# Kernel optimization log

Measured on AMD Instinct MI355X. Metric: run time of the kernel, lower is better.

Reference implementation:

```python
import jax, jax.numpy as jnp
import numpy as np

D = 256; HEADS = 8; DH = 32; LVLS = 3; PTS = 4; FF = 1024; FCD = 12544
SHAPES = ((100, 152), (50, 76), (25, 38))  # stride 8/16/32 maps for an 800x1216 image
INCH = (512, 1024, 2048)
N = 2; P_IMG = 1000


def sine_pos(h, w):
    # PositionEmbeddingSine, normalize=True, fully-valid mask
    eps = 1e-6; scale = 2.0 * np.pi
    y = jnp.cumsum(jnp.ones((h, w), jnp.float32), 0)
    x = jnp.cumsum(jnp.ones((h, w), jnp.float32), 1)
    y = y / (y[-1:, :] + eps) * scale
    x = x / (x[:, -1:] + eps) * scale
    dim_t = 10000.0 ** ((2.0 * (jnp.arange(128) // 2)).astype(jnp.float32) / 128.0)
    def inter(p):  # interleave sin/cos like torch.stack(...).flatten(3)
        return jnp.stack([jnp.sin(p[..., 0::2]), jnp.cos(p[..., 1::2])], -1).reshape(h, w, 128)
    return jnp.concatenate([inter(y[..., None] / dim_t), inter(x[..., None] / dim_t)], -1).reshape(h * w, D)


def bilinear(img, gx, gy):
    # F.grid_sample bilinear, align_corners=False, padding_mode='zeros'
    # img [C,H,W]; gx,gy in [-1,1] of any shape -> out [C, *gx.shape]
    C, H, W = img.shape
    x = ((gx + 1.0) * W - 1.0) * 0.5
    y = ((gy + 1.0) * H - 1.0) * 0.5
    x0 = jnp.floor(x); y0 = jnp.floor(y)
    wx = x - x0; wy = y - y0
    x0i = x0.astype(jnp.int32); y0i = y0.astype(jnp.int32)
    def g(xi, yi):
        ok = ((xi >= 0) & (xi < W) & (yi >= 0) & (yi < H)).astype(img.dtype)
        v = img[:, jnp.clip(yi, 0, H - 1), jnp.clip(xi, 0, W - 1)]
        return v * ok[None]
    return (g(x0i, y0i) * ((1 - wx) * (1 - wy))[None]
            + g(x0i + 1, y0i) * (wx * (1 - wy))[None]
            + g(x0i, y0i + 1) * ((1 - wx) * wy)[None]
            + g(x0i + 1, y0i + 1) * (wx * wy)[None])


def layernorm(x, g, b):
    mu = x.mean(-1, keepdims=True)
    var = ((x - mu) ** 2).mean(-1, keepdims=True)
    return (x - mu) / jnp.sqrt(var + 1e-5) * g + b


def _forward(feat0, feat1, feat2, point_coords, projw, projb, gng, gnb, level_embed,
             w_off, b_off, w_attn, b_attn, w_val, b_val, w_out, b_out,
             ln1_g, ln1_b, ln2_g, ln2_b, w_ff1, b_ff1, w_ff2, b_ff2, fc_w, fc_b):
    feats = (feat0, feat1, feat2)
    srcs = []; poss = []
    for l in range(LVLS):
        # input_proj: 1x1 conv + GroupNorm(32, 256)
        s = jnp.einsum('nchw,oc->nohw', feats[l], projw[l]) + projb[l][None, :, None, None]
        n, c, h, w = s.shape
        sg = s.reshape(n, 32, c // 32, h, w)
        mu = sg.mean((2, 3, 4), keepdims=True)
        var = ((sg - mu) ** 2).mean((2, 3, 4), keepdims=True)
        s = ((sg - mu) / jnp.sqrt(var + 1e-5)).reshape(n, c, h, w) * gng[l][None, :, None, None] + gnb[l][None, :, None, None]
        srcs.append(s.reshape(n, c, h * w).transpose(0, 2, 1))
        poss.append(sine_pos(h, w)[None] + level_embed[l][None, None, :])
    src = jnp.concatenate(srcs, 1)            # [N, Len, D]
    pos = jnp.concatenate(poss, 1)            # [1, Len, D] broadcast
    # reference points (valid_ratios == 1)
    refs = []
    for (h, w) in SHAPES:
        gy, gx = jnp.meshgrid((jnp.arange(h) + 0.5) / h, (jnp.arange(w) + 0.5) / w, indexing='ij')
        refs.append(jnp.stack([gx.ravel(), gy.ravel()], -1))
    ref = jnp.concatenate(refs, 0)            # [Len, 2] (x, y)
    Lq = src.shape[1]
    q = src + pos
    value = (src @ w_val.T + b_val).reshape(N, Lq, HEADS, DH)
    off = (q @ w_off.T + b_off).reshape(N, Lq, HEADS, LVLS, PTS, 2)
    aw = jax.nn.softmax((q @ w_attn.T + b_attn).reshape(N, Lq, HEADS, LVLS * PTS), -1).reshape(N, Lq, HEADS, LVLS, PTS)
    norm = jnp.array([[w, h] for (h, w) in SHAPES], jnp.float32)  # [L, 2] offset normalizer (W_, H_)
    locs = ref[None, :, None, None, None, :] + off / norm[None, None, None, :, None, :]  # [N,Lq,H,L,P,2]
    # MSDeformAttn core: per-level bilinear gather, accumulate weighted samples
    acc = jnp.zeros((N * HEADS, DH, Lq), src.dtype)
    start = 0
    for lvl, (h, w) in enumerate(SHAPES):
        v = value[:, start:start + h * w].transpose(0, 2, 3, 1).reshape(N * HEADS, DH, h, w)
        g = (2.0 * locs[:, :, :, lvl] - 1.0).transpose(0, 2, 1, 3, 4).reshape(N * HEADS, Lq, PTS, 2)
        s = jax.vmap(bilinear)(v, g[..., 0], g[..., 1])                 # [NH, DH, Lq, PTS]
        a = aw[:, :, :, lvl].transpose(0, 2, 1, 3).reshape(N * HEADS, 1, Lq, PTS)
        acc = acc + (s * a).sum(-1)
        start += h * w
    attn_out = acc.reshape(N, HEADS * DH, Lq).transpose(0, 2, 1) @ w_out.T + b_out
    x = layernorm(src + attn_out, ln1_g, ln1_b)
    ff = jax.nn.relu(x @ w_ff1.T + b_ff1) @ w_ff2.T + b_ff2
    x = layernorm(x + ff, ln2_g, ln2_b)
    # take level-0 tokens back to a feature map
    H0, W0 = SHAPES[0]
    mem = x.transpose(0, 2, 1)[:, :, :H0 * W0].reshape(N, D, H0, W0)
    # point_sample: grid_sample at 2*coords-1
    gpc = 2.0 * point_coords - 1.0
    pf = jax.vmap(bilinear)(mem, gpc[..., 0], gpc[..., 1])              # [N, D, P]
    pf = pf.transpose(0, 2, 1).reshape(N * P_IMG, D)
    # fc: Conv1d(256 -> 12544, k=1) + relu, then squeeze/permute
    return jax.nn.relu(pf @ fc_w.T + fc_b[None])


def setup_inputs() -> dict:
    key = jax.random.key(0)
    ki = iter(jax.random.split(key, 48))
    def rn(shape, scale):
        return jax.random.normal(next(ki), shape, jnp.float32) * scale
    d = {}
    d['feat0'] = jax.random.normal(next(ki), (N, 512, 100, 152), jnp.float32)
    d['feat1'] = jax.random.normal(next(ki), (N, 1024, 50, 76), jnp.float32)
    d['feat2'] = jax.random.normal(next(ki), (N, 2048, 25, 38), jnp.float32)
    d['point_coords'] = jax.random.uniform(next(ki), (N, P_IMG, 2), jnp.float32)
    d['gt_classes'] = jax.random.randint(next(ki), (N * P_IMG,), 0, 81)
    for l in range(LVLS):
        cin = INCH[l]
        d[f'proj{l}_w'] = rn((D, cin), 1.0 / np.sqrt(cin))
        d[f'proj{l}_b'] = jnp.zeros((D,), jnp.float32)
        d[f'gn{l}_g'] = jnp.ones((D,), jnp.float32)
        d[f'gn{l}_b'] = jnp.zeros((D,), jnp.float32)
    d['level_embed'] = rn((LVLS, D), 1.0)
    d['w_off'] = rn((HEADS * LVLS * PTS * 2, D), 0.01)
    d['b_off'] = rn((HEADS * LVLS * PTS * 2,), 0.2)
    d['w_attn'] = rn((HEADS * LVLS * PTS, D), 0.01)
    d['b_attn'] = jnp.zeros((HEADS * LVLS * PTS,), jnp.float32)
    d['w_val'] = rn((D, D), 1.0 / 16)
    d['b_val'] = jnp.zeros((D,), jnp.float32)
    d['w_out'] = rn((D, D), 1.0 / 16)
    d['b_out'] = jnp.zeros((D,), jnp.float32)
    d['ln1_g'] = jnp.ones((D,), jnp.float32); d['ln1_b'] = jnp.zeros((D,), jnp.float32)
    d['ln2_g'] = jnp.ones((D,), jnp.float32); d['ln2_b'] = jnp.zeros((D,), jnp.float32)
    d['w_ff1'] = rn((FF, D), 1.0 / 16); d['b_ff1'] = jnp.zeros((FF,), jnp.float32)
    d['w_ff2'] = rn((D, FF), 1.0 / 32); d['b_ff2'] = jnp.zeros((D,), jnp.float32)
    d['fc_w'] = rn((FCD, D), 1.0 / 16); d['fc_b'] = jnp.zeros((FCD,), jnp.float32)
    return d


def reference(feat0, feat1, feat2, point_coords, gt_classes,
              proj0_w, proj0_b, gn0_g, gn0_b, proj1_w, proj1_b, gn1_g, gn1_b,
              proj2_w, proj2_b, gn2_g, gn2_b, level_embed,
              w_off, b_off, w_attn, b_attn, w_val, b_val, w_out, b_out,
              ln1_g, ln1_b, ln2_g, ln2_b, w_ff1, b_ff1, w_ff2, b_ff2, fc_w, fc_b):
    out = _forward(feat0, feat1, feat2, point_coords,
                   (proj0_w, proj1_w, proj2_w), (proj0_b, proj1_b, proj2_b),
                   (gn0_g, gn1_g, gn2_g), (gn0_b, gn1_b, gn2_b), level_embed,
                   w_off, b_off, w_attn, b_attn, w_val, b_val, w_out, b_out,
                   ln1_g, ln1_b, ln2_g, ln2_b, w_ff1, b_ff1, w_ff2, b_ff2, fc_w, fc_b)
    return (out, gt_classes)
```

## Files before the change

### kernel.cpp

```cpp
#include <hip/hip_runtime.h>
#include <cstddef>
#include <cstdint>

#define D_MODEL 256
#define LQ 19950
#define NBATCH 2
#define NT (NBATCH*LQ)

typedef short  bf16x8 __attribute__((ext_vector_type(8)));
typedef float  f32x4  __attribute__((ext_vector_type(4)));
typedef unsigned short u16x8 __attribute__((ext_vector_type(8)));
typedef unsigned short u16x4 __attribute__((ext_vector_type(4)));

__device__ __forceinline__ unsigned short f2b(float f) {
  unsigned u = __float_as_uint(f);
  u += 0x7fff + ((u >> 16) & 1);
  return (unsigned short)(u >> 16);
}
__device__ __forceinline__ float b2f(unsigned short s) {
  return __uint_as_float(((unsigned)s) << 16);
}
__device__ __forceinline__ bf16x8 pack8(float4 a, float4 b) {
  bf16x8 r;
  r[0]=(short)f2b(a.x); r[1]=(short)f2b(a.y); r[2]=(short)f2b(a.z); r[3]=(short)f2b(a.w);
  r[4]=(short)f2b(b.x); r[5]=(short)f2b(b.y); r[6]=(short)f2b(b.z); r[7]=(short)f2b(b.w);
  return r;
}

#if __has_builtin(__builtin_amdgcn_global_load_lds)
#define HAVE_GLL 1
__device__ __forceinline__ void gload16(const void* g, void* lds_base_uniform) {
  __builtin_amdgcn_global_load_lds(
      (const __attribute__((address_space(1))) void*)g,
      (__attribute__((address_space(3))) void*)lds_base_uniform, 16, 0, 0);
}
#else
#define HAVE_GLL 0
#endif

template<bool ABF, int BMODE, bool CBF, bool RELU, bool ROWBIAS>
__global__ __launch_bounds__(256) void mgemm(
    const void* __restrict__ Av, const void* __restrict__ Bv,
    const float* __restrict__ bias, void* __restrict__ Cv,
    int M, int N, int K, int lda, int ldb, long sB, long sC, int zShift)
{
  __shared__ unsigned short As[64][72];
  __shared__ unsigned short Bs[64][72];
  const int tid = threadIdx.x;
  const int n0 = blockIdx.x * 64, m0 = blockIdx.y * 64;
  const int zb = blockIdx.z;
  const int n_b = zb >> zShift;
  const int kBase = (zb & ((1 << zShift) - 1)) * K;
  const int lane = tid & 63;
  const int wave = tid >> 6;
  const int l15 = lane & 15, q = lane >> 4;
  const int m_off = (wave >> 1) * 32, n_off = (wave & 1) * 32;
  f32x4 acc[2][2] = {};

  for (int k0 = kBase; k0 < kBase + K; k0 += 64) {
    {
      int row = tid >> 2, kc = (tid & 3) * 8;
      int gm = m0 + row;
      bf16x8 v0 = (bf16x8)0, v1 = (bf16x8)0;
      if (gm < M) {
        if constexpr (ABF) {
          const unsigned short* A = (const unsigned short*)Av;
          v0 = *(const bf16x8*)&A[(size_t)gm*lda + k0 + kc];
          v1 = *(const bf16x8*)&A[(size_t)gm*lda + k0 + kc + 32];
        } else {
          const float* A = (const float*)Av;
          const float* p = &A[(size_t)gm*lda + k0 + kc];
          v0 = pack8(*(const float4*)p,      *(const float4*)(p+4));
          v1 = pack8(*(const float4*)(p+32), *(const float4*)(p+36));
        }
      }
      *(bf16x8*)&As[row][kc]    = v0;
      *(bf16x8*)&As[row][kc+32] = v1;
    }
    if constexpr (BMODE == 1) {
      const float* Bp = (const float*)Bv + (size_t)n_b * sB;
      int kr = tid >> 3, nc = (tid & 7) * 8;
      #pragma unroll
      for (int half = 0; half < 2; ++half) {
        int kk = kr + half*32;
        const float* p = &Bp[(size_t)(k0+kk)*ldb + n0 + nc];
        float v[8];
        if (n0 + nc + 7 < N) {
          float2 a0 = *(const float2*)p,     a1 = *(const float2*)(p+2);
          float2 a2 = *(const float2*)(p+4), a3 = *(const float2*)(p+6);
          v[0]=a0.x; v[1]=a0.y; v[2]=a1.x; v[3]=a1.y;
          v[4]=a2.x; v[5]=a2.y; v[6]=a3.x; v[7]=a3.y;
        } else {
          #pragma unroll
          for (int i=0;i<8;++i) v[i] = (n0+nc+i < N) ? p[i] : 0.f;
        }
        #pragma unroll
        for (int i=0;i<8;++i) Bs[nc+i][kk] = f2b(v[i]);
      }
    }
    __syncthreads();
    #pragma unroll
    for (int s = 0; s < 2; ++s) {
      bf16x8 a0 = *(const bf16x8*)&As[m_off      + l15][s*32 + q*8];
      bf16x8 a1 = *(const bf16x8*)&As[m_off + 16 + l15][s*32 + q*8];
      bf16x8 b0 = *(const bf16x8*)&Bs[n_off      + l15][s*32 + q*8];
      bf16x8 b1 = *(const bf16x8*)&Bs[n_off + 16 + l15][s*32 + q*8];
      acc[0][0] = __builtin_amdgcn_mfma_f32_16x16x32_bf16(a0, b0, acc[0][0], 0,0,0);
      acc[0][1] = __builtin_amdgcn_mfma_f32_16x16x32_bf16(a0, b1, acc[0][1], 0,0,0);
      acc[1][0] = __builtin_amdgcn_mfma_f32_16x16x32_bf16(a1, b0, acc[1][0], 0,0,0);
      acc[1][1] = __builtin_amdgcn_mfma_f32_16x16x32_bf16(a1, b1, acc[1][1], 0,0,0);
    }
    __syncthreads();
  }
  float* Cf = (float*)Cv + (size_t)zb * sC;
  unsigned short* Cb = (unsigned short*)Cv + (size_t)zb * sC;
  #pragma unroll
  for (int r = 0; r < 2; ++r) {
    #pragma unroll
    for (int c = 0; c < 2; ++c) {
      #pragma unroll
      for (int v = 0; v < 4; ++v) {
        int gm = m0 + m_off + r*16 + q*4 + v;
        int gn = n0 + n_off + c*16 + l15;
        if (gm < M && gn < N) {
          float o = acc[r][c][v];
          if (bias) o += ROWBIAS ? bias[gm] : bias[gn];
          if (RELU) o = fmaxf(o, 0.f);
          if constexpr (CBF) Cb[(size_t)gm*N + gn] = f2b(o);
          else               Cf[(size_t)gm*N + gn] = o;
        }
      }
    }
  }
}

__global__ __launch_bounds__(256) void proj_reduce(
    const float* __restrict__ part, const float* __restrict__ bias,
    float* __restrict__ out, int HW, int S)
{
  int half = HW >> 1;
  int per_n = D_MODEL * half;
  int total = NBATCH * per_n;
  const float2* p2 = (const float2*)part;
  float2* o2 = (float2*)out;
  for (int i = blockIdx.x*256 + threadIdx.x; i < total; i += gridDim.x*256) {
    int n = i / per_n;
    int r = i - n*per_n;
    int o = r / half;
    int hw2 = r - o*half;
    float ax = 0.f, ay = 0.f;
    for (int s = 0; s < S; ++s) {
      float2 v = p2[((size_t)(n*S+s)*D_MODEL + o)*half + hw2];
      ax += v.x; ay += v.y;
    }
    float b = bias[o];
    o2[((size_t)n*D_MODEL + o)*half + hw2] = make_float2(ax+b, ay+b);
  }
}

template<bool CBF, bool RELU>
__global__ __launch_bounds__(512) void gemm_bb(
    const unsigned short* __restrict__ A, const unsigned short* __restrict__ B,
    const float* __restrict__ bias, void* __restrict__ Cv,
    int M, int N, int K, int lda, int ldb)
{
  __shared__ unsigned short SA[2][8192];
  __shared__ unsigned short SB[2][8192];
  const int tid = threadIdx.x;
  const int lane = tid & 63, wave = tid >> 6;
  const int nwg = gridDim.x * gridDim.y;
  const int flat = blockIdx.y * gridDim.x + blockIdx.x;
  const int qn = nwg >> 3, rr = nwg & 7;
  const int xcd = flat & 7, lid = flat >> 3;
  const int swz = (xcd < rr ? xcd*(qn+1) : rr*(qn+1) + (xcd-rr)*qn) + lid;
  const int n0 = (swz % gridDim.x) * 128;
  const int m0 = (swz / gridDim.x) * 128;

  const int l15 = lane & 15, q = lane >> 4;
  const int m_off = (wave >> 2) * 64, n_off = (wave & 3) * 32;
  const int sr = lane >> 3;
  const int ssl = (lane & 7) ^ sr;
  const int rs = l15 & 7;
  f32x4 acc[4][2] = {};

  const int nt = K >> 6;

  #pragma unroll
  for (int c = 0; c < 2; ++c) {
    int ch = wave*2 + c;
    const unsigned short* ga = A + (size_t)(m0 + ch*8 + sr)*lda + ssl*8;
    const unsigned short* gb = B + (size_t)(n0 + ch*8 + sr)*ldb + ssl*8;
#if HAVE_GLL
    gload16(ga, &SA[0][ch*512]);
    gload16(gb, &SB[0][ch*512]);
#else
    *(bf16x8*)&SA[0][ch*512 + lane*8] = *(const bf16x8*)ga;
    *(bf16x8*)&SB[0][ch*512 + lane*8] = *(const bf16x8*)gb;
#endif
  }

  for (int t = 0; t < nt - 1; ++t) {
    {
      int k1 = (t + 1) << 6;
      #pragma unroll
      for (int c = 0; c < 2; ++c) {
        int ch = wave*2 + c;
        const unsigned short* ga = A + (size_t)(m0 + ch*8 + sr)*lda + k1 + ssl*8;
        const unsigned short* gb = B + (size_t)(n0 + ch*8 + sr)*ldb + k1 + ssl*8;
#if HAVE_GLL
        gload16(ga, &SA[(t+1)&1][ch*512]);
        gload16(gb, &SB[(t+1)&1][ch*512]);
#else
        *(bf16x8*)&SA[(t+1)&1][ch*512 + lane*8] = *(const bf16x8*)ga;
        *(bf16x8*)&SB[(t+1)&1][ch*512 + lane*8] = *(const bf16x8*)gb;
#endif
      }
    }
#if HAVE_GLL
    asm volatile("s_waitcnt vmcnt(4)" ::: "memory");
    __builtin_amdgcn_s_barrier();
#else
    __syncthreads();
#endif
    {
      const unsigned short* sa = SA[t&1];
      const unsigned short* sb = SB[t&1];
      #pragma unroll
      for (int s = 0; s < 2; ++s) {
        int ps = ((s*4 + q) ^ rs) * 8;
        bf16x8 af[4], bfr[2];
        #pragma unroll
        for (int i = 0; i < 4; ++i)
          af[i] = *(const bf16x8*)&sa[(m_off + i*16 + l15)*64 + ps];
        #pragma unroll
        for (int j = 0; j < 2; ++j)
          bfr[j] = *(const bf16x8*)&sb[(n_off + j*16 + l15)*64 + ps];
        #pragma unroll
        for (int i = 0; i < 4; ++i)
          #pragma unroll
          for (int j = 0; j < 2; ++j)
            acc[i][j] = __builtin_amdgcn_mfma_f32_16x16x32_bf16(af[i], bfr[j], acc[i][j], 0,0,0);
      }
    }
#if HAVE_GLL
    __builtin_amdgcn_s_barrier();
#else
    __syncthreads();
#endif
  }
#if HAVE_GLL
  asm volatile("s_waitcnt vmcnt(0)" ::: "memory");
  __builtin_amdgcn_s_barrier();
#else
  __syncthreads();
#endif
  {
    const unsigned short* sa = SA[(nt-1)&1];
    const unsigned short* sb = SB[(nt-1)&1];
    #pragma unroll
    for (int s = 0; s < 2; ++s) {
      int ps = ((s*4 + q) ^ rs) * 8;
      bf16x8 af[4], bfr[2];
      #pragma unroll
      for (int i = 0; i < 4; ++i)
        af[i] = *(const bf16x8*)&sa[(m_off + i*16 + l15)*64 + ps];
      #pragma unroll
      for (int j = 0; j < 2; ++j)
        bfr[j] = *(const bf16x8*)&sb[(n_off + j*16 + l15)*64 + ps];
      #pragma unroll
      for (int i = 0; i < 4; ++i)
        #pragma unroll
        for (int j = 0; j < 2; ++j)
          acc[i][j] = __builtin_amdgcn_mfma_f32_16x16x32_bf16(af[i], bfr[j], acc[i][j], 0,0,0);
    }
  }

  float* Cf = (float*)Cv;
  unsigned short* Cb = (unsigned short*)Cv;
  #pragma unroll
  for (int i = 0; i < 4; ++i) {
    #pragma unroll
    for (int j = 0; j < 2; ++j) {
      #pragma unroll
      for (int v = 0; v < 4; ++v) {
        int gm = m0 + m_off + i*16 + q*4 + v;
        int gn = n0 + n_off + j*16 + l15;
        if (gm < M && gn < N) {
          float o = acc[i][j][v];
          if (bias) o += bias[gn];
          if (RELU) o = fmaxf(o, 0.f);
          if constexpr (CBF) Cb[(size_t)gm*N + gn] = f2b(o);
          else               Cf[(size_t)gm*N + gn] = o;
        }
      }
    }
  }
}

__global__ __launch_bounds__(512) void gemm_vo(
    const unsigned short* __restrict__ Asrc, const unsigned short* __restrict__ Aq,
    const unsigned short* __restrict__ Bv,   const unsigned short* __restrict__ Bo,
    const float* __restrict__ bias_v, const float* __restrict__ bias_o,
    unsigned short* __restrict__ Cv, unsigned short* __restrict__ Co, int M)
{
  __shared__ unsigned short SA[2][8192];
  __shared__ unsigned short SB[2][8192];
  const int tid = threadIdx.x;
  const int lane = tid & 63, wave = tid >> 6;
  const int nwg = gridDim.x * gridDim.y;
  const int flat = blockIdx.y * gridDim.x + blockIdx.x;
  const int qn = nwg >> 3, rr = nwg & 7;
  const int xcd = flat & 7, lid = flat >> 3;
  const int swz = (xcd < rr ? xcd*(qn+1) : rr*(qn+1) + (xcd-rr)*qn) + lid;
  const int colid = swz % gridDim.x;
  const int m0 = (swz / gridDim.x) * 128;

  const unsigned short* A; const unsigned short* B;
  const float* bias; unsigned short* C; int N, n0;
  if (colid < 2) { A = Asrc; B = Bv; bias = bias_v; C = Cv; N = 256; n0 = colid*128; }
  else           { A = Aq;   B = Bo; bias = bias_o; C = Co; N = 288; n0 = (colid-2)*128; }

  const int l15 = lane & 15, q = lane >> 4;
  const int m_off = (wave >> 2) * 64, n_off = (wave & 3) * 32;
  const int sr = lane >> 3;
  const int ssl = (lane & 7) ^ sr;
  const int rs = l15 & 7;
  f32x4 acc[4][2] = {};
  const int nt = 4;

  #pragma unroll
  for (int c = 0; c < 2; ++c) {
    int ch = wave*2 + c;
    const unsigned short* ga = A + (size_t)(m0 + ch*8 + sr)*256 + ssl*8;
    const unsigned short* gb = B + (size_t)(n0 + ch*8 + sr)*256 + ssl*8;
#if HAVE_GLL
    gload16(ga, &SA[0][ch*512]);
    gload16(gb, &SB[0][ch*512]);
#else
    *(bf16x8*)&SA[0][ch*512 + lane*8] = *(const bf16x8*)ga;
    *(bf16x8*)&SB[0][ch*512 + lane*8] = *(const bf16x8*)gb;
#endif
  }

  for (int t = 0; t < nt - 1; ++t) {
    {
      int k1 = (t + 1) << 6;
      #pragma unroll
      for (int c = 0; c < 2; ++c) {
        int ch = wave*2 + c;
        const unsigned short* ga = A + (size_t)(m0 + ch*8 + sr)*256 + k1 + ssl*8;
        const unsigned short* gb = B + (size_t)(n0 + ch*8 + sr)*256 + k1 + ssl*8;
#if HAVE_GLL
        gload16(ga, &SA[(t+1)&1][ch*512]);
        gload16(gb, &SB[(t+1)&1][ch*512]);
#else
        *(bf16x8*)&SA[(t+1)&1][ch*512 + lane*8] = *(const bf16x8*)ga;
        *(bf16x8*)&SB[(t+1)&1][ch*512 + lane*8] = *(const bf16x8*)gb;
#endif
      }
    }
#if HAVE_GLL
    asm volatile("s_waitcnt vmcnt(4)" ::: "memory");
    __builtin_amdgcn_s_barrier();
#else
    __syncthreads();
#endif
    {
      const unsigned short* sa = SA[t&1];
      const unsigned short* sb = SB[t&1];
      #pragma unroll
      for (int s = 0; s < 2; ++s) {
        int ps = ((s*4 + q) ^ rs) * 8;
        bf16x8 af[4], bfr[2];
        #pragma unroll
        for (int i = 0; i < 4; ++i)
          af[i] = *(const bf16x8*)&sa[(m_off + i*16 + l15)*64 + ps];
        #pragma unroll
        for (int j = 0; j < 2; ++j)
          bfr[j] = *(const bf16x8*)&sb[(n_off + j*16 + l15)*64 + ps];
        #pragma unroll
        for (int i = 0; i < 4; ++i)
          #pragma unroll
          for (int j = 0; j < 2; ++j)
            acc[i][j] = __builtin_amdgcn_mfma_f32_16x16x32_bf16(af[i], bfr[j], acc[i][j], 0,0,0);
      }
    }
#if HAVE_GLL
    __builtin_amdgcn_s_barrier();
#else
    __syncthreads();
#endif
  }
#if HAVE_GLL
  asm volatile("s_waitcnt vmcnt(0)" ::: "memory");
  __builtin_amdgcn_s_barrier();
#else
  __syncthreads();
#endif
  {
    const unsigned short* sa = SA[(nt-1)&1];
    const unsigned short* sb = SB[(nt-1)&1];
    #pragma unroll
    for (int s = 0; s < 2; ++s) {
      int ps = ((s*4 + q) ^ rs) * 8;
      bf16x8 af[4], bfr[2];
      #pragma unroll
      for (int i = 0; i < 4; ++i)
        af[i] = *(const bf16x8*)&sa[(m_off + i*16 + l15)*64 + ps];
      #pragma unroll
      for (int j = 0; j < 2; ++j)
        bfr[j] = *(const bf16x8*)&sb[(n_off + j*16 + l15)*64 + ps];
      #pragma unroll
      for (int i = 0; i < 4; ++i)
        #pragma unroll
        for (int j = 0; j < 2; ++j)
          acc[i][j] = __builtin_amdgcn_mfma_f32_16x16x32_bf16(af[i], bfr[j], acc[i][j], 0,0,0);
    }
  }

  #pragma unroll
  for (int i = 0; i < 4; ++i) {
    #pragma unroll
    for (int j = 0; j < 2; ++j) {
      #pragma unroll
      for (int v = 0; v < 4; ++v) {
        int gm = m0 + m_off + i*16 + q*4 + v;
        int gn = n0 + n_off + j*16 + l15;
        if (gm < M && gn < N) {
          float o = acc[i][j][v] + bias[gn];
          C[(size_t)gm*N + gn] = f2b(o);
        }
      }
    }
  }
}

struct W7 { const float* src[7]; unsigned short* dst[7]; int nv[7]; };
__global__ __launch_bounds__(256) void wconv(W7 w)
{
  int s = blockIdx.y;
  const float4* src = (const float4*)w.src[s];
  unsigned short* dst = w.dst[s];
  int n = w.nv[s];
  for (int i = blockIdx.x*256 + threadIdx.x; i < n; i += gridDim.x*256) {
    float4 v = src[i];
    u16x4 o = { f2b(v.x), f2b(v.y), f2b(v.z), f2b(v.w) };
    *(u16x4*)(dst + (size_t)i*4) = o;
  }
}

__global__ __launch_bounds__(288) void biascat(
    const float* __restrict__ b_off, const float* __restrict__ b_attn,
    float* __restrict__ out)
{
  int i = threadIdx.x;
  out[i] = (i < 192) ? b_off[i] : b_attn[i - 192];
}

__global__ __launch_bounds__(256) void gn_partial(
    const float* __restrict__ s, float* __restrict__ partials, int HW)
{
  int g = blockIdx.x, n = blockIdx.y, c = blockIdx.z;
  const float4* base = (const float4*)(s + ((size_t)n*D_MODEL + g*8) * HW);
  int nvec = (8*HW) >> 2;
  float sum = 0.f, sq = 0.f;
  for (int j = c*256 + threadIdx.x; j < nvec; j += 2048) {
    float4 v = base[j];
    sum += v.x+v.y+v.z+v.w;
    sq  += v.x*v.x+v.y*v.y+v.z*v.z+v.w*v.w;
  }
  #pragma unroll
  for (int m=32;m;m>>=1){ sum += __shfl_xor(sum,m,64); sq += __shfl_xor(sq,m,64); }
  __shared__ float s1[4], s2[4];
  int w = threadIdx.x >> 6;
  if ((threadIdx.x & 63) == 0) { s1[w]=sum; s2[w]=sq; }
  __syncthreads();
  if (threadIdx.x == 0) {
    partials[(((size_t)n*32+g)*8 + c)*2]     = s1[0]+s1[1]+s1[2]+s1[3];
    partials[(((size_t)n*32+g)*8 + c)*2 + 1] = s2[0]+s2[1]+s2[2]+s2[3];
  }
}

__global__ __launch_bounds__(256) void gn_apply(
    const float* __restrict__ s, const float* __restrict__ partials,
    const float* __restrict__ gw, const float* __restrict__ gb,
    float* __restrict__ src, int HW, int loff)
{
  __shared__ float T[32][33];
  __shared__ float smu[4], srs[4];
  int tx = threadIdx.x & 31, ty = threadIdx.x >> 5;
  int hw0 = blockIdx.x*32, o0 = blockIdx.y*32, n = blockIdx.z;
  if (threadIdx.x < 4) {
    int g = (o0 >> 3) + threadIdx.x;
    float S = 0.f, Q = 0.f;
    #pragma unroll
    for (int c = 0; c < 8; ++c) {
      S += partials[(((size_t)n*32+g)*8 + c)*2];
      Q += partials[(((size_t)n*32+g)*8 + c)*2 + 1];
    }
    float inv = 1.f/(float)(8*HW);
    float mu = S*inv;
    float var = Q*inv - mu*mu;
    smu[threadIdx.x] = mu;
    srs[threadIdx.x] = rsqrtf(var + 1e-5f);
  }
  __syncthreads();
  const float* base = s + (size_t)n*D_MODEL*HW;
  #pragma unroll
  for (int it=0; it<4; ++it) {
    int ol = ty + it*8;
    int o = o0 + ol;
    int hw = hw0 + tx;
    float v = 0.f;
    if (hw < HW) {
      v = (base[(size_t)o*HW + hw] - smu[ol>>3])*srs[ol>>3]*gw[o] + gb[o];
    }
    T[ol][tx] = v;
  }
  __syncthreads();
  #pragma unroll
  for (int it=0; it<4; ++it) {
    int tl = ty + it*8;
    int tok = hw0 + tl;
    if (tok < HW) {
      src[((size_t)n*LQ + loff + tok)*D_MODEL + o0 + tx] = T[tx][tl];
    }
  }
}

__global__ __launch_bounds__(256) void compute_q(
    const float* __restrict__ src, const float* __restrict__ level_embed,
    unsigned short* __restrict__ q, unsigned short* __restrict__ srcbf)
{
  int row = blockIdx.x;
  int d = threadIdx.x;
  int tok = (row >= LQ) ? row - LQ : row;
  int H, W, lvl, i, j;
  if (tok < 15200)      { lvl=0; H=100; W=152; int hw=tok;        i=hw/152; j=hw-i*152; }
  else if (tok < 19000) { lvl=1; H=50;  W=76;  int hw=tok-15200;  i=hw/76;  j=hw-i*76;  }
  else                  { lvl=2; H=25;  W=38;  int hw=tok-19000;  i=hw/38;  j=hw-i*38;  }
  const float TWO_PI = 6.28318530717958647692f;
  float yv = (float)(i+1) / ((float)H + 1e-6f) * TWO_PI;
  float xv = (float)(j+1) / ((float)W + 1e-6f) * TWO_PI;
  int m = (d & 127) >> 1;
  float invt = __expf((float)m * -0.14391156516f);
  float ang = ((d < 128) ? yv : xv) * invt;
  float pe = (d & 1) ? __cosf(ang) : __sinf(ang);
  size_t idx = (size_t)row*D_MODEL + d;
  float sv = src[idx];
  q[idx] = f2b(sv + pe + level_embed[lvl*D_MODEL + d]);
  srcbf[idx] = f2b(sv);
}

__global__ __launch_bounds__(256) void deform_sample(
    const unsigned short* __restrict__ value, const unsigned short* __restrict__ offaw,
    unsigned short* __restrict__ accb)
{
  int idx = blockIdx.x*256 + threadIdx.x;
  if (idx >= NT*8*4) return;
  int quarter = idx & 3;
  int h = (idx >> 2) & 7;
  int row = idx >> 5;
  int n = (row >= LQ) ? 1 : 0;
  int tok = row - n*LQ;

  float bxs0, bxs1, bxs2, bys0, bys1, bys2;
  if (tok < 15200) {
    int ti = tok/152, tj = tok - ti*152;
    float bx = tj + 0.5f, by = ti + 0.5f;
    bxs0 = bx - 0.5f;         bys0 = by - 0.5f;
    bxs1 = bx*0.5f - 0.5f;    bys1 = by*0.5f - 0.5f;
    bxs2 = bx*0.25f - 0.5f;   bys2 = by*0.25f - 0.5f;
  } else if (tok < 19000) {
    int hw = tok - 15200; int ti = hw/76, tj = hw - ti*76;
    float bx = tj + 0.5f, by = ti + 0.5f;
    bxs0 = bx*2.f - 0.5f;     bys0 = by*2.f - 0.5f;
    bxs1 = bx - 0.5f;         bys1 = by - 0.5f;
    bxs2 = bx*0.5f - 0.5f;    bys2 = by*0.5f - 0.5f;
  } else {
    int hw = tok - 19000; int ti = hw/38, tj = hw - ti*38;
    float bx = tj + 0.5f, by = ti + 0.5f;
    bxs0 = bx*4.f - 0.5f;     bys0 = by*4.f - 0.5f;
    bxs1 = bx*2.f - 0.5f;     bys1 = by*2.f - 0.5f;
    bxs2 = bx - 0.5f;         bys2 = by - 0.5f;
  }
  const float bxs[3] = {bxs0, bxs1, bxs2};
  const float bys[3] = {bys0, bys1, bys2};

  const unsigned short* offr = offaw + (size_t)row*288 + h*24;
  const unsigned short* awr  = offaw + (size_t)row*288 + 192 + h*12;
  float off[24];
  {
    u16x8 o0 = *(const u16x8*)offr;
    u16x8 o1 = *(const u16x8*)(offr+8);
    u16x8 o2 = *(const u16x8*)(offr+16);
    #pragma unroll
    for (int c=0;c<8;++c){ off[c]=b2f(o0[c]); off[8+c]=b2f(o1[c]); off[16+c]=b2f(o2[c]); }
  }
  float lg[12];
  {
    u16x4 a0 = *(const u16x4*)awr;
    u16x4 a1 = *(const u16x4*)(awr+4);
    u16x4 a2 = *(const u16x4*)(awr+8);
    #pragma unroll
    for (int c=0;c<4;++c){ lg[c]=b2f(a0[c]); lg[4+c]=b2f(a1[c]); lg[8+c]=b2f(a2[c]); }
  }
  float mx = -1e30f;
  #pragma unroll
  for (int i=0;i<12;++i) mx = fmaxf(mx, lg[i]);
  float ssum = 0.f;
  #pragma unroll
  for (int i=0;i<12;++i){ lg[i] = __expf(lg[i]-mx); ssum += lg[i]; }
  float sinv = 1.f/ssum;

  float acc[8] = {0.f,0.f,0.f,0.f,0.f,0.f,0.f,0.f};
  const int HH[3]={100,50,25}, WW[3]={152,76,38}, OO[3]={0,15200,19000};
  int chbase = h*32 + quarter*8;
  #pragma unroll
  for (int lvl=0; lvl<3; ++lvl) {
    const int H=HH[lvl], W=WW[lvl], lo=OO[lvl];
    const unsigned short* vbase = value + ((size_t)(n*LQ + lo)*D_MODEL) + chbase;
    #pragma unroll
    for (int p=0; p<4; ++p) {
      float ox = off[lvl*8 + p*2];
      float oy = off[lvl*8 + p*2 + 1];
      float a  = lg[lvl*4 + p] * sinv;
      float x = bxs[lvl] + ox;
      float y = bys[lvl] + oy;
      float x0f = floorf(x), y0f = floorf(y);
      float wx = x - x0f, wy = y - y0f;
      int x0 = (int)x0f, y0 = (int)y0f;
      float w00 = (1.f-wx)*(1.f-wy)*a, w10 = wx*(1.f-wy)*a;
      float w01 = (1.f-wx)*wy*a,       w11 = wx*wy*a;
      if ((unsigned)x0 < (unsigned)(W-1) && (unsigned)y0 < (unsigned)(H-1)) {
        const unsigned short* b00 = vbase + (size_t)(y0*W + x0)*D_MODEL;
        u16x8 v00 = *(const u16x8*)b00;
        u16x8 v10 = *(const u16x8*)(b00 + D_MODEL);
        u16x8 v01 = *(const u16x8*)(b00 + W*D_MODEL);
        u16x8 v11 = *(const u16x8*)(b00 + W*D_MODEL + D_MODEL);
        #pragma unroll
        for (int c=0;c<8;++c)
          acc[c] += w00*b2f(v00[c]) + w10*b2f(v10[c]) + w01*b2f(v01[c]) + w11*b2f(v11[c]);
      } else {
        float tw[4] = { w00, w10, w01, w11 };
        #pragma unroll
        for (int t=0; t<4; ++t) {
          int xi = x0 + (t & 1), yi = y0 + (t >> 1);
          if (xi >= 0 && xi < W && yi >= 0 && yi < H) {
            const float w = tw[t];
            const unsigned short* vr = vbase + (size_t)(yi*W + xi)*D_MODEL;
            u16x8 v = *(const u16x8*)vr;
            #pragma unroll
            for (int jj=0;jj<8;++jj) acc[jj] += w * b2f(v[jj]);
          }
        }
      }
    }
  }
  unsigned short* o = accb + (size_t)row*D_MODEL + chbase;
  u16x8 ov;
  #pragma unroll
  for (int jj=0;jj<8;++jj) ov[jj] = f2b(acc[jj]);
  *(u16x8*)o = ov;
}

template<bool EMITBF>
__global__ __launch_bounds__(256) void ln_add(
    const float* __restrict__ A, const float* __restrict__ B,
    const float* __restrict__ g, const float* __restrict__ b,
    float* __restrict__ out, unsigned short* __restrict__ outbf, int rows)
{
  int wid = (blockIdx.x * 256 + threadIdx.x) >> 6;
  int lane = threadIdx.x & 63;
  if (wid >= rows) return;
  size_t base = (size_t)wid * D_MODEL;
  float4 va = *(const float4*)&A[base + lane*4];
  float4 vb = *(const float4*)&B[base + lane*4];
  float v[4] = {va.x+vb.x, va.y+vb.y, va.z+vb.z, va.w+vb.w};
  float s = v[0]+v[1]+v[2]+v[3];
  #pragma unroll
  for (int m=32; m; m>>=1) s += __shfl_xor(s, m, 64);
  float mu = s * (1.f/256.f);
  float qq = 0.f;
  #pragma unroll
  for (int i=0;i<4;++i){ float d=v[i]-mu; qq += d*d; }
  #pragma unroll
  for (int m=32; m; m>>=1) qq += __shfl_xor(qq, m, 64);
  float rstd = rsqrtf(qq*(1.f/256.f) + 1e-5f);
  float o[4];
  #pragma unroll
  for (int i=0;i<4;++i){
    int d = lane*4+i;
    o[i] = (v[i]-mu)*rstd*g[d] + b[d];
  }
  *(float4*)&out[base + lane*4] = make_float4(o[0],o[1],o[2],o[3]);
  if constexpr (EMITBF) {
    u16x4 ob = { f2b(o[0]), f2b(o[1]), f2b(o[2]), f2b(o[3]) };
    *(u16x4*)&outbf[base + lane*4] = ob;
  }
}

__global__ __launch_bounds__(256) void point_sample(
    const float* __restrict__ x2, const float* __restrict__ pc,
    unsigned short* __restrict__ pf)
{
  int pidx = blockIdx.x;
  int n = pidx / 1000;
  float px = pc[(size_t)pidx*2], py = pc[(size_t)pidx*2+1];
  float x = ((2.f*px)*152.f - 1.f)*0.5f;
  float y = ((2.f*py)*100.f - 1.f)*0.5f;
  float x0f=floorf(x), y0f=floorf(y);
  float wx=x-x0f, wy=y-y0f;
  int x0=(int)x0f, y0=(int)y0f;
  int d = threadIdx.x;
  float accv = 0.f;
  #pragma unroll
  for (int t=0;t<4;++t) {
    int xi = x0 + (t&1), yi = y0 + (t>>1);
    float w = ((t&1)?wx:(1.f-wx)) * ((t>>1)?wy:(1.f-wy));
    if (xi>=0 && xi<152 && yi>=0 && yi<100) {
      accv += w * x2[((size_t)(n*LQ + yi*152 + xi))*D_MODEL + d];
    }
  }
  pf[(size_t)pidx*D_MODEL + d] = f2b(accv);
}

__global__ void copy_gt(const int* __restrict__ gt, float* __restrict__ out, int nels)
{
  int i = blockIdx.x*256 + threadIdx.x;
  if (i < nels) out[i] = (float)gt[i];
}

extern "C" void kernel_launch(void* const* d_in, const int* in_sizes, int n_in,
                              void* d_out, int out_size, void* d_ws, size_t ws_size,
                              hipStream_t stream)
{
  const float* feat[3]  = {(const float*)d_in[0], (const float*)d_in[1], (const float*)d_in[2]};
  const float* pc       = (const float*)d_in[3];
  const int*   gt       = (const int*)d_in[4];
  const float* projw[3] = {(const float*)d_in[5],  (const float*)d_in[9],  (const float*)d_in[13]};
  const float* projb[3] = {(const float*)d_in[6],  (const float*)d_in[10], (const float*)d_in[14]};
  const float* gng[3]   = {(const float*)d_in[7],  (const float*)d_in[11], (const float*)d_in[15]};
  const float* gnb[3]   = {(const float*)d_in[8],  (const float*)d_in[12], (const float*)d_in[16]};
  const float* level_embed = (const float*)d_in[17];
  const float* w_off  = (const float*)d_in[18];
  const float* b_off  = (const float*)d_in[19];
  const float* w_attn = (const float*)d_in[20];
  const float* b_attn = (const float*)d_in[21];
  const float* w_val  = (const float*)d_in[22];
  const float* b_val  = (const float*)d_in[23];
  const float* w_out  = (const float*)d_in[24];
  const float* b_out  = (const float*)d_in[25];
  const float* ln1g   = (const float*)d_in[26];
  const float* ln1b   = (const float*)d_in[27];
  const float* ln2g   = (const float*)d_in[28];
  const float* ln2b   = (const float*)d_in[29];
  const float* wff1   = (const float*)d_in[30];
  const float* bff1   = (const float*)d_in[31];
  const float* wff2   = (const float*)d_in[32];
  const float* bff2   = (const float*)d_in[33];
  const float* fcw    = (const float*)d_in[34];
  const float* fcb    = (const float*)d_in[35];

  float* ws    = (float*)d_ws;
  float* s_tmp = ws;
  unsigned short* q_b     = (unsigned short*)(s_tmp + 10214400);
  unsigned short* value_b = q_b + 10214400;
  float* srcb  = (float*)(value_b + 10214400);
  float* xreg  = srcb + 10214400;
  unsigned short* offaw   = (unsigned short*)(xreg + 10214400);
  unsigned short* wbf     = offaw + 11491200;
  float* partials = (float*)(wbf + 3940352);
  float* boffaw   = partials + 1024;

  unsigned short* wv_bf  = wbf;
  unsigned short* wof_bf = wbf + 65536;
  unsigned short* wat_bf = wbf + 114688;
  unsigned short* wou_bf = wbf + 139264;
  unsigned short* wf1_bf = wbf + 204800;
  unsigned short* wf2_bf = wbf + 466944;
  unsigned short* wfc_bf = wbf + 729088;

  float* kpart = xreg;
  unsigned short* src_bf = (unsigned short*)xreg;
  unsigned short* acc_b = q_b;
  unsigned short* xb_bf = offaw;
  unsigned short* hbuf  = (unsigned short*)s_tmp;
  unsigned short* pf    = value_b;
  float* ybuf = srcb;
  float* x2   = s_tmp;

  W7 w7;
  w7.src[0]=w_val;  w7.dst[0]=wv_bf;  w7.nv[0]=65536/4;
  w7.src[1]=w_off;  w7.dst[1]=wof_bf; w7.nv[1]=49152/4;
  w7.src[2]=w_attn; w7.dst[2]=wat_bf; w7.nv[2]=24576/4;
  w7.src[3]=w_out;  w7.dst[3]=wou_bf; w7.nv[3]=65536/4;
  w7.src[4]=wff1;   w7.dst[4]=wf1_bf; w7.nv[4]=262144/4;
  w7.src[5]=wff2;   w7.dst[5]=wf2_bf; w7.nv[5]=262144/4;
  w7.src[6]=fcw;    w7.dst[6]=wfc_bf; w7.nv[6]=3211264/4;
  wconv<<<dim3(512, 7), 256, 0, stream>>>(w7);
  biascat<<<1, 288, 0, stream>>>(b_off, b_attn, boffaw);

  const int HWs[3]  = {15200, 3800, 950};
  const int Cins[3] = {512, 1024, 2048};
  const int LOFF[3] = {0, 15200, 19000};
  const int ZSH[3]  = {0, 1, 2};

  for (int l = 0; l < 3; ++l) {
    int HW = HWs[l], K = Cins[l];
    int S = 1 << ZSH[l];
    int KC = K / S;
    if (S == 1) {
      mgemm<false,1,false,false,true><<<dim3((HW+63)/64, 4, NBATCH), 256, 0, stream>>>(
          projw[l], feat[l], projb[l], s_tmp, D_MODEL, HW, KC, K, HW,
          (long)K*HW, (long)D_MODEL*HW, 0);
    } else {
      mgemm<false,1,false,false,true><<<dim3((HW+63)/64, 4, NBATCH*S), 256, 0, stream>>>(
          projw[l], feat[l], nullptr, kpart, D_MODEL, HW, KC, K, HW,
          (long)K*HW, (long)D_MODEL*HW, ZSH[l]);
      int total2 = NBATCH * D_MODEL * (HW >> 1);
      int gr = (total2 + 255) / 256; if (gr > 2048) gr = 2048;
      proj_reduce<<<gr, 256, 0, stream>>>(kpart, projb[l], s_tmp, HW, S);
    }
    gn_partial<<<dim3(32, NBATCH, 8), 256, 0, stream>>>(s_tmp, partials, HW);
    gn_apply<<<dim3((HW+31)/32, 8, NBATCH), 256, 0, stream>>>(
        s_tmp, partials, gng[l], gnb[l], srcb, HW, LOFF[l]);
  }

  compute_q<<<NT, 256, 0, stream>>>(srcb, level_embed, q_b, src_bf);

  int gm128 = (NT + 127) / 128;
  gemm_vo<<<dim3(5, gm128), 512, 0, stream>>>(
      src_bf, q_b, wv_bf, wof_bf, b_val, boffaw, value_b, offaw, NT);

  deform_sample<<<(NT*8*4 + 255)/256, 256, 0, stream>>>(value_b, offaw, acc_b);

  gemm_bb<false,false><<<dim3(2, gm128), 512, 0, stream>>>(
      acc_b, wou_bf, b_out, s_tmp, NT, 256, 256, 256, 256);
  ln_add<true><<<(NT+3)/4, 256, 0, stream>>>(srcb, s_tmp, ln1g, ln1b, xreg, xb_bf, NT);

  gemm_bb<true,true><<<dim3(8, gm128), 512, 0, stream>>>(
      xb_bf, wf1_bf, bff1, hbuf, NT, 1024, 256, 256, 256);
  gemm_bb<false,false><<<dim3(2, gm128), 512, 0, stream>>>(
      hbuf, wf2_bf, bff2, ybuf, NT, 256, 1024, 1024, 1024);

  ln_add<false><<<(NT+3)/4, 256, 0, stream>>>(xreg, ybuf, ln2g, ln2b, x2, nullptr, NT);

  point_sample<<<2000, 256, 0, stream>>>(x2, pc, pf);
  gemm_bb<false,true><<<dim3(12544/128, (2000+127)/128), 512, 0, stream>>>(
      pf, wfc_bf, fcb, (float*)d_out, 2000, 12544, 256, 256, 256);
  copy_gt<<<8, 256, 0, stream>>>(gt, (float*)d_out + (size_t)2000*12544, 2000);
}
```

Before: 509.7 us.

## Route level-0/1 input projections through bf16 gemm_bb with transposed features

Levels 0 and 1 of the input projection now convert their 1x1-conv weights to bf16 and transpose the NCHW features into token-major bf16 with a new tconv kernel. This lets them reuse the 128x128 MFMA gemm_bb with a row-bias option, batching both images into one wide GEMM instead of the mgemm path. The projection output layout changes to channel-major across batch [256, N*HW], so the GroupNorm and reduce kernels are rewritten to index it. The cost is an extra transpose and conversion pass over large feature maps, plus bf16 rounding of the projection inputs.

```diff
diff --git a/kernel.cpp b/kernel.cpp
--- a/kernel.cpp
+++ b/kernel.cpp
@@ -134,7 +134,7 @@
   }
 }
 
-__global__ __launch_bounds__(256) void proj_reduce(
+__global__ __launch_bounds__(256) void proj_reduce2(
     const float* __restrict__ part, const float* __restrict__ bias,
     float* __restrict__ out, int HW, int S)
 {
@@ -154,11 +154,11 @@
       ax += v.x; ay += v.y;
     }
     float b = bias[o];
-    o2[((size_t)n*D_MODEL + o)*half + hw2] = make_float2(ax+b, ay+b);
-  }
-}
-
-template<bool CBF, bool RELU>
+    o2[(size_t)o*HW + (size_t)n*half + hw2] = make_float2(ax+b, ay+b);
+  }
+}
+
+template<bool CBF, bool RELU, bool RB>
 __global__ __launch_bounds__(512) void gemm_bb(
     const unsigned short* __restrict__ A, const unsigned short* __restrict__ B,
     const float* __restrict__ bias, void* __restrict__ Cv,
@@ -287,7 +287,7 @@
         int gn = n0 + n_off + j*16 + l15;
         if (gm < M && gn < N) {
           float o = acc[i][j][v];
-          if (bias) o += bias[gn];
+          if (bias) o += RB ? bias[gm] : bias[gn];
           if (RELU) o = fmaxf(o, 0.f);
           if constexpr (CBF) Cb[(size_t)gm*N + gn] = f2b(o);
           else               Cf[(size_t)gm*N + gn] = o;
@@ -435,8 +435,33 @@
   }
 }
 
-struct W7 { const float* src[7]; unsigned short* dst[7]; int nv[7]; };
-__global__ __launch_bounds__(256) void wconv(W7 w)
+__global__ __launch_bounds__(256) void tconv(
+    const float* __restrict__ feat, unsigned short* __restrict__ featT,
+    int C, int HW)
+{
+  __shared__ float T[32][33];
+  int hw0 = blockIdx.x*32, c0 = blockIdx.y*32, n = blockIdx.z;
+  const float* base = feat + (size_t)n*C*HW;
+  int tx = threadIdx.x & 31, ty = threadIdx.x >> 5;
+  #pragma unroll
+  for (int it=0; it<4; ++it) {
+    int c = c0 + ty + it*8;
+    int hw = hw0 + tx;
+    T[ty+it*8][tx] = (hw < HW) ? base[(size_t)c*HW + hw] : 0.f;
+  }
+  __syncthreads();
+  #pragma unroll
+  for (int it=0; it<4; ++it) {
+    int tl = ty + it*8;
+    int tok = hw0 + tl;
+    if (tok < HW) {
+      featT[((size_t)n*HW + tok)*C + c0 + tx] = f2b(T[tx][tl]);
+    }
+  }
+}
+
+struct W9 { const float* src[9]; unsigned short* dst[9]; int nv[9]; };
+__global__ __launch_bounds__(256) void wconv(W9 w)
 {
   int s = blockIdx.y;
   const float4* src = (const float4*)w.src[s];
@@ -457,32 +482,35 @@
   out[i] = (i < 192) ? b_off[i] : b_attn[i - 192];
 }
 
-__global__ __launch_bounds__(256) void gn_partial(
-    const float* __restrict__ s, float* __restrict__ partials, int HW)
+__global__ __launch_bounds__(256) void gn_partial2(
+    const float* __restrict__ s2, float* __restrict__ partials, int HW)
 {
   int g = blockIdx.x, n = blockIdx.y, c = blockIdx.z;
-  const float4* base = (const float4*)(s + ((size_t)n*D_MODEL + g*8) * HW);
-  int nvec = (8*HW) >> 2;
+  int NHW = HW*2;
+  int nvec2 = HW >> 1;
+  int total = nvec2*8;
   float sum = 0.f, sq = 0.f;
-  for (int j = c*256 + threadIdx.x; j < nvec; j += 2048) {
-    float4 v = base[j];
-    sum += v.x+v.y+v.z+v.w;
-    sq  += v.x*v.x+v.y*v.y+v.z*v.z+v.w*v.w;
+  for (int j = c*256 + threadIdx.x; j < total; j += 2048) {
+    int r = j / nvec2;
+    int v = j - r*nvec2;
+    const float2 x = *(const float2*)(s2 + (size_t)(g*8+r)*NHW + (size_t)n*HW + v*2);
+    sum += x.x + x.y;
+    sq  += x.x*x.x + x.y*x.y;
   }
   #pragma unroll
   for (int m=32;m;m>>=1){ sum += __shfl_xor(sum,m,64); sq += __shfl_xor(sq,m,64); }
-  __shared__ float s1[4], s2[4];
+  __shared__ float s1[4], s2s[4];
   int w = threadIdx.x >> 6;
-  if ((threadIdx.x & 63) == 0) { s1[w]=sum; s2[w]=sq; }
+  if ((threadIdx.x & 63) == 0) { s1[w]=sum; s2s[w]=sq; }
   __syncthreads();
   if (threadIdx.x == 0) {
     partials[(((size_t)n*32+g)*8 + c)*2]     = s1[0]+s1[1]+s1[2]+s1[3];
-    partials[(((size_t)n*32+g)*8 + c)*2 + 1] = s2[0]+s2[1]+s2[2]+s2[3];
-  }
-}
-
-__global__ __launch_bounds__(256) void gn_apply(
-    const float* __restrict__ s, const float* __restrict__ partials,
+    partials[(((size_t)n*32+g)*8 + c)*2 + 1] = s2s[0]+s2s[1]+s2s[2]+s2s[3];
+  }
+}
+
+__global__ __launch_bounds__(256) void gn_apply2(
+    const float* __restrict__ s2, const float* __restrict__ partials,
     const float* __restrict__ gw, const float* __restrict__ gb,
     float* __restrict__ src, int HW, int loff)
 {
@@ -490,6 +518,7 @@
   __shared__ float smu[4], srs[4];
   int tx = threadIdx.x & 31, ty = threadIdx.x >> 5;
   int hw0 = blockIdx.x*32, o0 = blockIdx.y*32, n = blockIdx.z;
+  int NHW = HW*2;
   if (threadIdx.x < 4) {
     int g = (o0 >> 3) + threadIdx.x;
     float S = 0.f, Q = 0.f;
@@ -505,7 +534,6 @@
     srs[threadIdx.x] = rsqrtf(var + 1e-5f);
   }
   __syncthreads();
-  const float* base = s + (size_t)n*D_MODEL*HW;
   #pragma unroll
   for (int it=0; it<4; ++it) {
     int ol = ty + it*8;
@@ -513,7 +541,7 @@
     int hw = hw0 + tx;
     float v = 0.f;
     if (hw < HW) {
-      v = (base[(size_t)o*HW + hw] - smu[ol>>3])*srs[ol>>3]*gw[o] + gb[o];
+      v = (s2[(size_t)o*NHW + (size_t)n*HW + hw] - smu[ol>>3])*srs[ol>>3]*gw[o] + gb[o];
     }
     T[ol][tx] = v;
   }
@@ -770,7 +798,7 @@
   float* xreg  = srcb + 10214400;
   unsigned short* offaw   = (unsigned short*)(xreg + 10214400);
   unsigned short* wbf     = offaw + 11491200;
-  float* partials = (float*)(wbf + 3940352);
+  float* partials = (float*)(wbf + 4333568);
   float* boffaw   = partials + 1024;
 
   unsigned short* wv_bf  = wbf;
@@ -780,7 +808,10 @@
   unsigned short* wf1_bf = wbf + 204800;
   unsigned short* wf2_bf = wbf + 466944;
   unsigned short* wfc_bf = wbf + 729088;
-
+  unsigned short* wp0_bf = wbf + 3940352;
+  unsigned short* wp1_bf = wbf + 4071424;
+
+  unsigned short* featT = q_b;
   float* kpart = xreg;
   unsigned short* src_bf = (unsigned short*)xreg;
   unsigned short* acc_b = q_b;
@@ -790,41 +821,45 @@
   float* ybuf = srcb;
   float* x2   = s_tmp;
 
-  W7 w7;
-  w7.src[0]=w_val;  w7.dst[0]=wv_bf;  w7.nv[0]=65536/4;
-  w7.src[1]=w_off;  w7.dst[1]=wof_bf; w7.nv[1]=49152/4;
-  w7.src[2]=w_attn; w7.dst[2]=wat_bf; w7.nv[2]=24576/4;
-  w7.src[3]=w_out;  w7.dst[3]=wou_bf; w7.nv[3]=65536/4;
-  w7.src[4]=wff1;   w7.dst[4]=wf1_bf; w7.nv[4]=262144/4;
-  w7.src[5]=wff2;   w7.dst[5]=wf2_bf; w7.nv[5]=262144/4;
-  w7.src[6]=fcw;    w7.dst[6]=wfc_bf; w7.nv[6]=3211264/4;
-  wconv<<<dim3(512, 7), 256, 0, stream>>>(w7);
+  W9 w9;
+  w9.src[0]=w_val;    w9.dst[0]=wv_bf;  w9.nv[0]=65536/4;
+  w9.src[1]=w_off;    w9.dst[1]=wof_bf; w9.nv[1]=49152/4;
+  w9.src[2]=w_attn;   w9.dst[2]=wat_bf; w9.nv[2]=24576/4;
+  w9.src[3]=w_out;    w9.dst[3]=wou_bf; w9.nv[3]=65536/4;
+  w9.src[4]=wff1;     w9.dst[4]=wf1_bf; w9.nv[4]=262144/4;
+  w9.src[5]=wff2;     w9.dst[5]=wf2_bf; w9.nv[5]=262144/4;
+  w9.src[6]=fcw;      w9.dst[6]=wfc_bf; w9.nv[6]=3211264/4;
+  w9.src[7]=projw[0]; w9.dst[7]=wp0_bf; w9.nv[7]=131072/4;
+  w9.src[8]=projw[1]; w9.dst[8]=wp1_bf; w9.nv[8]=262144/4;
+  wconv<<<dim3(512, 9), 256, 0, stream>>>(w9);
   biascat<<<1, 288, 0, stream>>>(b_off, b_attn, boffaw);
 
-  const int HWs[3]  = {15200, 3800, 950};
-  const int Cins[3] = {512, 1024, 2048};
-  const int LOFF[3] = {0, 15200, 19000};
-  const int ZSH[3]  = {0, 1, 2};
-
-  for (int l = 0; l < 3; ++l) {
-    int HW = HWs[l], K = Cins[l];
-    int S = 1 << ZSH[l];
-    int KC = K / S;
-    if (S == 1) {
-      mgemm<false,1,false,false,true><<<dim3((HW+63)/64, 4, NBATCH), 256, 0, stream>>>(
-          projw[l], feat[l], projb[l], s_tmp, D_MODEL, HW, KC, K, HW,
-          (long)K*HW, (long)D_MODEL*HW, 0);
-    } else {
-      mgemm<false,1,false,false,true><<<dim3((HW+63)/64, 4, NBATCH*S), 256, 0, stream>>>(
-          projw[l], feat[l], nullptr, kpart, D_MODEL, HW, KC, K, HW,
-          (long)K*HW, (long)D_MODEL*HW, ZSH[l]);
-      int total2 = NBATCH * D_MODEL * (HW >> 1);
-      int gr = (total2 + 255) / 256; if (gr > 2048) gr = 2048;
-      proj_reduce<<<gr, 256, 0, stream>>>(kpart, projb[l], s_tmp, HW, S);
-    }
-    gn_partial<<<dim3(32, NBATCH, 8), 256, 0, stream>>>(s_tmp, partials, HW);
-    gn_apply<<<dim3((HW+31)/32, 8, NBATCH), 256, 0, stream>>>(
-        s_tmp, partials, gng[l], gnb[l], srcb, HW, LOFF[l]);
+  {
+    tconv<<<dim3(475, 16, 2), 256, 0, stream>>>(feat[0], featT, 512, 15200);
+    gemm_bb<false,false,true><<<dim3(238, 2), 512, 0, stream>>>(
+        wp0_bf, featT, projb[0], s_tmp, 256, 30400, 512, 512, 512);
+    gn_partial2<<<dim3(32, 2, 8), 256, 0, stream>>>(s_tmp, partials, 15200);
+    gn_apply2<<<dim3(475, 8, 2), 256, 0, stream>>>(
+        s_tmp, partials, gng[0], gnb[0], srcb, 15200, 0);
+  }
+  {
+    tconv<<<dim3(119, 32, 2), 256, 0, stream>>>(feat[1], featT, 1024, 3800);
+    gemm_bb<false,false,true><<<dim3(60, 2), 512, 0, stream>>>(
+        wp1_bf, featT, projb[1], s_tmp, 256, 7600, 1024, 1024, 1024);
+    gn_partial2<<<dim3(32, 2, 8), 256, 0, stream>>>(s_tmp, partials, 3800);
+    gn_apply2<<<dim3(119, 8, 2), 256, 0, stream>>>(
+        s_tmp, partials, gng[1], gnb[1], srcb, 3800, 15200);
+  }
+  {
+    mgemm<false,1,false,false,true><<<dim3(15, 4, 8), 256, 0, stream>>>(
+        projw[2], feat[2], nullptr, kpart, D_MODEL, 950, 512, 2048, 950,
+        (long)2048*950, (long)D_MODEL*950, 2);
+    int total2 = NBATCH * D_MODEL * (950 >> 1);
+    int gr = (total2 + 255) / 256; if (gr > 2048) gr = 2048;
+    proj_reduce2<<<gr, 256, 0, stream>>>(kpart, projb[2], s_tmp, 950, 4);
+    gn_partial2<<<dim3(32, 2, 8), 256, 0, stream>>>(s_tmp, partials, 950);
+    gn_apply2<<<dim3(30, 8, 2), 256, 0, stream>>>(
+        s_tmp, partials, gng[2], gnb[2], srcb, 950, 19000);
   }
 
   compute_q<<<NT, 256, 0, stream>>>(srcb, level_embed, q_b, src_bf);
@@ -835,19 +870,19 @@
 
   deform_sample<<<(NT*8*4 + 255)/256, 256, 0, stream>>>(value_b, offaw, acc_b);
 
-  gemm_bb<false,false><<<dim3(2, gm128), 512, 0, stream>>>(
+  gemm_bb<false,false,false><<<dim3(2, gm128), 512, 0, stream>>>(
       acc_b, wou_bf, b_out, s_tmp, NT, 256, 256, 256, 256);
   ln_add<true><<<(NT+3)/4, 256, 0, stream>>>(srcb, s_tmp, ln1g, ln1b, xreg, xb_bf, NT);
 
-  gemm_bb<true,true><<<dim3(8, gm128), 512, 0, stream>>>(
+  gemm_bb<true,true,false><<<dim3(8, gm128), 512, 0, stream>>>(
       xb_bf, wf1_bf, bff1, hbuf, NT, 1024, 256, 256, 256);
-  gemm_bb<false,false><<<dim3(2, gm128), 512, 0, stream>>>(
+  gemm_bb<false,false,false><<<dim3(2, gm128), 512, 0, stream>>>(
       hbuf, wf2_bf, bff2, ybuf, NT, 256, 1024, 1024, 1024);
 
   ln_add<false><<<(NT+3)/4, 256, 0, stream>>>(xreg, ybuf, ln2g, ln2b, x2, nullptr, NT);
 
   point_sample<<<2000, 256, 0, stream>>>(x2, pc, pf);
-  gemm_bb<false,true><<<dim3(12544/128, (2000+127)/128), 512, 0, stream>>>(
+  gemm_bb<false,true,false><<<dim3(12544/128, (2000+127)/128), 512, 0, stream>>>(
       pf, wfc_bf, fcb, (float*)d_out, 2000, 12544, 256, 256, 256);
   copy_gt<<<8, 256, 0, stream>>>(gt, (float*)d_out + (size_t)2000*12544, 2000);
 }
```

Measured after the change: 496.1 us. -2.7%, faster.
